# Performance work log

Hardware: AMD Instinct MI355X
Metric: run time of the kernel (lower is better)

## Reference

```python
import jax, jax.numpy as jnp
import numpy as np

GAMMA = 1.4
EX = jnp.array([1.0, 0.0], dtype=jnp.float32)
EY = jnp.array([0.0, 1.0], dtype=jnp.float32)


def _mlp(x, Ws, bs):
    h = x
    for W, b in zip(Ws[:-1], bs[:-1]):
        h = jnp.tanh(h @ W + b)
    return h @ Ws[-1] + bs[-1]


def setup_inputs() -> dict:
    key = jax.random.key(0)
    ks = jax.random.split(key, 24)
    N, NB = 32768, 4096
    inp = {}
    dom = jnp.array([1.5, 1.0], dtype=jnp.float32)
    inp['x_train'] = jax.random.uniform(ks[0], (N, 2), dtype=jnp.float32) * dom
    inp['x_inlet'] = jax.random.uniform(ks[1], (NB, 2), dtype=jnp.float32) * dom
    inp['U_inlet'] = jax.random.normal(ks[2], (NB, 4), dtype=jnp.float32)
    inp['x_base'] = jax.random.uniform(ks[3], (NB, 2), dtype=jnp.float32) * dom
    inp['x_top'] = jax.random.uniform(ks[4], (NB, 2), dtype=jnp.float32) * dom
    inp['x_slipNormal'] = jax.random.uniform(ks[5], (NB, 2), dtype=jnp.float32) * dom
    dims = [2, 128, 128, 128, 128, 4]
    for i in range(5):
        fan_in = dims[i]
        inp[f'W{i}'] = jax.random.normal(ks[6 + i], (dims[i], dims[i + 1]), dtype=jnp.float32) / jnp.sqrt(jnp.float32(fan_in))
        inp[f'b{i}'] = jnp.zeros((dims[i + 1],), dtype=jnp.float32)
    d2 = [2, 64, 64, 1]
    for i in range(3):
        inp[f'V{i}'] = jax.random.normal(ks[12 + i], (d2[i], d2[i + 1]), dtype=jnp.float32) / jnp.sqrt(jnp.float32(d2[i]))
        inp[f'c{i}'] = jnp.zeros((d2[i + 1],), dtype=jnp.float32)
    return inp


def reference(x_train, x_inlet, U_inlet, x_base, x_top, x_slipNormal,
              W0, b0, W1, b1, W2, b2, W3, b3, W4, b4,
              V0, c0, V1, c1, V2, c2):
    Ws = [W0, W1, W2, W3, W4]
    bs = [b0, b1, b2, b3, b4]
    Vs = [V0, V1, V2]
    cs = [c0, c1, c2]

    def fields(xy):
        # per-point: returns [U1..U4, f1..f4, g1..g4] (12,)
        rho, p, u, v = _mlp(xy, Ws, bs)
        E = p / (GAMMA - 1.0) + 0.5 * rho * (u * u + v * v)
        return jnp.stack([
            rho, rho * u, rho * v, E,                               # U
            rho * u, rho * u * u + p, rho * u * v, u * (E + p),     # f (x-flux)
            rho * v, rho * u * v, rho * v * v + p, v * (E + p)])    # g (y-flux)

    def dUx(xy):
        return jax.jvp(fields, (xy,), (EX,))[1][:4]

    def dUy(xy):
        return jax.jvp(fields, (xy,), (EY,))[1][:4]

    def point_residual(xy):
        _, dx = jax.jvp(fields, (xy,), (EX,))   # x-derivs of all 12 fields
        _, dy = jax.jvp(fields, (xy,), (EY,))   # y-derivs
        U_xx = jax.jvp(dUx, (xy,), (EX,))[1]    # second derivs (fwd-over-fwd)
        U_yy = jax.jvp(dUy, (xy,), (EY,))[1]
        mu = 0.01 * _mlp(xy, Vs, cs)[0] ** 2
        res = dx[4:8] + dy[8:12] - mu * (U_xx + U_yy)  # (4,)
        return res, mu

    res, mu = jax.vmap(point_residual)(x_train)  # res: (N,4), mu: (N,)
    physics = jnp.sum(jnp.mean(res ** 2, axis=0))  # r1+r2+r3+r4

    out_in = _mlp(x_inlet, Ws, bs)
    inlet = jnp.sum(jnp.mean((out_in - U_inlet) ** 2, axis=0))

    base = jnp.mean(_mlp(x_base, Ws, bs)[:, 3] ** 2)
    top = jnp.mean(_mlp(x_top, Ws, bs)[:, 3] ** 2)

    ang = -jnp.pi / 18.0
    o = _mlp(x_slipNormal, Ws, bs)
    slip = jnp.mean((-o[:, 2] * jnp.sin(ang) + o[:, 3] * jnp.cos(ang)) ** 2)

    total = physics + 10.0 * (inlet + base + top + slip) + 0.1 * jnp.mean(mu ** 2)
    return total
```

## Files before the change

kernel.cpp:

```cpp
#include <hip/hip_runtime.h>

#define NTRAIN 32768
#define NBDY   4096
#define PHYS_BLOCKS (NTRAIN / 16)
#define BDY_BLOCKS  512

typedef _Float16 f16x8 __attribute__((ext_vector_type(8)));
typedef __fp16   fp16x2 __attribute__((ext_vector_type(2)));
typedef float    f32x4 __attribute__((ext_vector_type(4)));

union FragU { uint4 q; f16x8 b; _Float16 e[8]; };
union F4  { float4 v; float f[4]; };
union U2h { _Float16 e[4]; uint2 d; };
union H2  { fp16x2 h; _Float16 e[2]; unsigned int u; };

__device__ __forceinline__ float fast_tanh(float z) {
    float e = __expf(2.0f * z);
    return 1.0f - 2.0f * __builtin_amdgcn_rcpf(e + 1.0f);
}

__device__ __forceinline__ unsigned int pk2(float a, float b) {
    H2 r; r.h = __builtin_amdgcn_cvt_pkrtz(a, b);
    return r.u;
}

__global__ __launch_bounds__(256) void pack_w_kernel(
    const float* __restrict__ W1, const float* __restrict__ W2,
    const float* __restrict__ W3, const float* __restrict__ V1,
    const float* __restrict__ W4,
    unsigned short* __restrict__ wsU, float* __restrict__ out)
{
    int b = blockIdx.x;
    if (b < 24) {
        int mat = b >> 3, rb = b & 7;
        const float* W = (mat == 0) ? W1 : (mat == 1) ? W2 : W3;
        unsigned int* hiU = (unsigned int*)(wsU + mat * 32768);
        unsigned int* loU = hiU + 8192;
        int n   = threadIdx.x & 127;
        int pr0 = threadIdx.x >> 7;
        #pragma unroll
        for (int it = 0; it < 4; it++) {
            int pr = pr0 + 2 * it;
            int k  = rb * 16 + pr * 2;
            float v0 = W[k * 128 + n];
            float v1 = W[(k + 1) * 128 + n];
            H2 hh, ll;
            hh.e[0] = (_Float16)v0;
            hh.e[1] = (_Float16)v1;
            ll.e[0] = (_Float16)(v0 - (float)hh.e[0]);
            ll.e[1] = (_Float16)(v1 - (float)hh.e[1]);
            int base = ((n >> 4) * 4 + (k >> 5)) * 64 + ((k >> 3) & 3) * 16 + (n & 15);
            int uoff = base * 4 + ((k & 7) >> 1);
            hiU[uoff] = hh.u;
            loU[uoff] = ll.u;
        }
    } else if (b == 24) {
        unsigned int* hiU = (unsigned int*)(wsU + 98304);
        int n   = threadIdx.x & 63;
        int pr0 = threadIdx.x >> 6;
        #pragma unroll
        for (int it = 0; it < 8; it++) {
            int pr = pr0 + 4 * it;
            int k  = pr * 2;
            float v0 = V1[k * 64 + n];
            float v1 = V1[(k + 1) * 64 + n];
            H2 hh;
            hh.e[0] = (_Float16)v0;
            hh.e[1] = (_Float16)v1;
            int base = ((n >> 4) * 2 + (k >> 5)) * 64 + ((k >> 3) & 3) * 16 + (n & 15);
            hiU[base * 4 + ((k & 7) >> 1)] = hh.u;
        }
        if (threadIdx.x == 0) out[0] = 0.f;
    } else {
        _Float16* hi = (_Float16*)(wsU + 102400);
        _Float16* lo = hi + 2048;
        int u4 = threadIdx.x;
        int lane = u4 & 63, ks = u4 >> 6;
        int m  = lane & 15;
        int kb = ks * 32 + ((lane >> 4) << 3);
        FragU fh, fl;
        #pragma unroll
        for (int j = 0; j < 8; j++) {
            float v = (m < 4) ? W4[(kb + j) * 4 + m] : 0.f;
            _Float16 h = (_Float16)v;
            fh.e[j] = h;
            fl.e[j] = (_Float16)(v - (float)h);
        }
        *(uint4*)(hi + u4 * 8) = fh.q;
        *(uint4*)(lo + u4 * 8) = fl.q;
    }
}

__global__ __launch_bounds__(256, 6) void fused_kernel(
    const float* __restrict__ xt,
    const float* __restrict__ x_inlet, const float* __restrict__ U_inlet,
    const float* __restrict__ x_base,  const float* __restrict__ x_top,
    const float* __restrict__ x_slip,
    const float* __restrict__ W0, const float* __restrict__ b0,
    const float* __restrict__ W1, const float* __restrict__ b1,
    const float* __restrict__ W2, const float* __restrict__ b2,
    const float* __restrict__ W3, const float* __restrict__ b3,
    const float* __restrict__ W4, const float* __restrict__ b4,
    const float* __restrict__ V0, const float* __restrict__ c0,
    const float* __restrict__ V1, const float* __restrict__ c1,
    const float* __restrict__ V2, const float* __restrict__ c2,
    const unsigned short* __restrict__ wsU,
    float* __restrict__ out)
{
    __shared__ float SM[5008];
    const int t = threadIdx.x;
    const int wv   = t >> 6;
    const int lane = t & 63;
    const int nn   = lane & 15;
    const int q    = lane >> 4;

    if (blockIdx.x < PHYS_BLOCKS) {
        unsigned short* AhU = (unsigned short*)SM;
        float* OUTF  = SM + 4352;
        float* MUV   = SM + 4608;
        float* BIASF = SM + 4624;
        unsigned short* MUhU  = AhU;
        unsigned short* MU2hU = AhU + 1152;

        const int p = t >> 4;
        const int c = t & 15;

        const int ptIdx = blockIdx.x * 16 + p;
        const float2 xy = *(const float2*)(xt + ptIdx * 2);
        const float x = xy.x, y = xy.y;

        if (t < 128) {
            BIASF[t]       = b1[t];
            BIASF[128 + t] = b2[t];
            BIASF[256 + t] = b3[t];
        }

        {
            F4 va, vb, cc;
            va.v = *(const float4*)(V0 + c * 4);
            vb.v = *(const float4*)(V0 + 64 + c * 4);
            cc.v = *(const float4*)(c0 + c * 4);
            float t0 = fast_tanh(x * va.f[0] + y * vb.f[0] + cc.f[0]);
            float t1 = fast_tanh(x * va.f[1] + y * vb.f[1] + cc.f[1]);
            float t2 = fast_tanh(x * va.f[2] + y * vb.f[2] + cc.f[2]);
            float t3 = fast_tanh(x * va.f[3] + y * vb.f[3] + cc.f[3]);
            uint2 d = make_uint2(pk2(t0, t1), pk2(t2, t3));
            *(uint2*)(MUhU + p * 72 + c * 4) = d;
        }
        __syncthreads();

        {
            f32x4 macc = {0.f, 0.f, 0.f, 0.f};
            #pragma unroll
            for (int ks = 0; ks < 2; ks++) {
                FragU mh, vh;
                mh.q = *(const uint4*)(MUhU + nn * 72 + ks * 32 + q * 8);
                vh.q = *(const uint4*)(wsU + 98304 + (((wv * 2 + ks) * 64 + lane) << 3));
                macc = __builtin_amdgcn_mfma_f32_16x16x32_f16(vh.b, mh.b, macc, 0, 0, 0);
            }
            int u2base = wv * 16 + q * 4;
            F4 cv; cv.v = *(const float4*)(c1 + u2base);
            float t0 = fast_tanh(macc[0] + cv.f[0]);
            float t1 = fast_tanh(macc[1] + cv.f[1]);
            float t2 = fast_tanh(macc[2] + cv.f[2]);
            float t3 = fast_tanh(macc[3] + cv.f[3]);
            uint2 d = make_uint2(pk2(t0, t1), pk2(t2, t3));
            *(uint2*)(MU2hU + nn * 72 + u2base) = d;
        }
        __syncthreads();

        if (t < 64) {
            int pt = t & 15, kg = t >> 4;
            float partial = 0.f;
            int base = pt * 72 + kg * 16;
            #pragma unroll
            for (int g = 0; g < 4; g++) {
                U2h hh;
                hh.d = *(const uint2*)(MU2hU + base + g * 4);
                F4 w; w.v = *(const float4*)(V2 + kg * 16 + g * 4);
                #pragma unroll
                for (int e = 0; e < 4; e++)
                    partial += (float)hh.e[e] * w.f[e];
            }
            partial += __shfl_down(partial, 32);
            partial += __shfl_down(partial, 16);
            if (t < 16) {
                float s = partial + c2[0];
                MUV[t] = 0.01f * s * s;
            }
        }
        __syncthreads();

        {
            float vals[4][8];
            #pragma unroll
            for (int j = 0; j < 8; j++) {
                int u = c * 8 + j;
                float w0 = W0[u], w1 = W0[128 + u];
                float zv = x * w0 + y * w1 + b0[u];
                float tt = fast_tanh(zv);
                float s2 = 1.f - tt * tt;
                float m2 = -2.f * tt * s2;
                vals[0][j] = tt;
                vals[1][j] = s2 * w0;
                vals[2][j] = s2 * w1;
                vals[3][j] = m2 * (w0 * w0 + w1 * w1);
            }
            #pragma unroll
            for (int s = 0; s < 4; s++) {
                uint4 d = make_uint4(pk2(vals[s][0], vals[s][1]),
                                     pk2(vals[s][2], vals[s][3]),
                                     pk2(vals[s][4], vals[s][5]),
                                     pk2(vals[s][6], vals[s][7]));
                *(uint4*)(AhU + (s * 16 + p) * 136 + c * 8) = d;
            }
        }
        __syncthreads();

        #pragma unroll 1
        for (int l = 0; l < 3; l++) {
            const unsigned short* WpL = wsU + l * 32768;
            f32x4 acc[2][4];
            #pragma unroll
            for (int i = 0; i < 2; i++)
                #pragma unroll
                for (int s = 0; s < 4; s++) {
                    acc[i][s][0] = 0.f; acc[i][s][1] = 0.f;
                    acc[i][s][2] = 0.f; acc[i][s][3] = 0.f;
                }
            #pragma unroll
            for (int ks = 0; ks < 4; ks++) {
                FragU bh[4];
                #pragma unroll
                for (int s = 0; s < 4; s++)
                    bh[s].q = *(const uint4*)(AhU + (s * 16 + nn) * 136 + ks * 32 + q * 8);
                FragU wh[2], wl[2];
                #pragma unroll
                for (int i = 0; i < 2; i++) {
                    const unsigned short* base =
                        WpL + ((((2 * wv + i) * 4 + ks) * 64 + lane) << 3);
                    wh[i].q = *(const uint4*)base;
                    wl[i].q = *(const uint4*)(base + 16384);
                }
                #pragma unroll
                for (int i = 0; i < 2; i++)
                    #pragma unroll
                    for (int s = 0; s < 4; s++) {
                        acc[i][s] = __builtin_amdgcn_mfma_f32_16x16x32_f16(
                            wh[i].b, bh[s].b, acc[i][s], 0, 0, 0);
                        acc[i][s] = __builtin_amdgcn_mfma_f32_16x16x32_f16(
                            wl[i].b, bh[s].b, acc[i][s], 0, 0, 0);
                    }
            }
            __syncthreads();
            #pragma unroll
            for (int i = 0; i < 2; i++) {
                int ubase = (2 * wv + i) * 16 + q * 4;
                F4 bv; bv.v = *(const float4*)&BIASF[l * 128 + ubase];
                float vals[4][4];
                #pragma unroll
                for (int r = 0; r < 4; r++) {
                    float z  = acc[i][0][r] + bv.f[r];
                    float zx = acc[i][1][r], zy = acc[i][2][r];
                    float zl = acc[i][3][r];
                    float tt = fast_tanh(z);
                    float s2 = 1.f - tt * tt;
                    float m2 = -2.f * tt * s2;
                    vals[0][r] = tt;
                    vals[1][r] = s2 * zx;
                    vals[2][r] = s2 * zy;
                    vals[3][r] = s2 * zl + m2 * (zx * zx + zy * zy);
                }
                #pragma unroll
                for (int s = 0; s < 4; s++) {
                    uint2 d = make_uint2(pk2(vals[s][0], vals[s][1]),
                                         pk2(vals[s][2], vals[s][3]));
                    *(uint2*)(AhU + (s * 16 + nn) * 136 + ubase) = d;
                }
            }
            __syncthreads();
        }

        {
            const unsigned short* W4p = wsU + 102400;
            f32x4 a4 = {0.f, 0.f, 0.f, 0.f};
            #pragma unroll
            for (int ks = 0; ks < 4; ks++) {
                FragU bh, wh, wl;
                bh.q = *(const uint4*)(AhU + (wv * 16 + nn) * 136 + ks * 32 + q * 8);
                const unsigned short* base = W4p + ((ks * 64 + lane) << 3);
                wh.q = *(const uint4*)base;
                wl.q = *(const uint4*)(base + 2048);
                a4 = __builtin_amdgcn_mfma_f32_16x16x32_f16(wh.b, bh.b, a4, 0, 0, 0);
                a4 = __builtin_amdgcn_mfma_f32_16x16x32_f16(wl.b, bh.b, a4, 0, 0, 0);
            }
            if (q == 0) {
                float4 o = make_float4(a4[0], a4[1], a4[2], a4[3]);
                if (wv == 0) {
                    o.x += b4[0]; o.y += b4[1]; o.z += b4[2]; o.w += b4[3];
                }
                *(float4*)&OUTF[(wv * 16 + nn) * 4] = o;
            }
        }
        __syncthreads();

        float contrib = 0.f;
        if (t < 16) {
            const int pp = t;
            const float* V   = &OUTF[(0  + pp) * 4];
            const float* DX  = &OUTF[(16 + pp) * 4];
            const float* DY  = &OUTF[(32 + pp) * 4];
            const float* LAP = &OUTF[(48 + pp) * 4];
            float r = V[0],  P = V[1],  u = V[2],  v = V[3];
            float rx = DX[0], Px = DX[1], ux = DX[2], vx = DX[3];
            float ry = DY[0], Py = DY[1], uy = DY[2], vy = DY[3];
            float rl = LAP[0], Pl = LAP[1], ul = LAP[2], vl = LAP[3];
            const float GI = 2.5f;

            float q2 = u * u + v * v;
            float E  = P * GI + 0.5f * r * q2;
            float Ex = Px * GI + 0.5f * rx * q2 + r * (u * ux + v * vx);
            float Ey = Py * GI + 0.5f * ry * q2 + r * (u * uy + v * vy);
            float EpP = E + P;

            float f1x = rx * u + r * ux;
            float f2x = rx * u * u + 2.f * r * u * ux + Px;
            float f3x = rx * u * v + r * ux * v + r * u * vx;
            float f4x = ux * EpP + u * (Ex + Px);

            float g1y = ry * v + r * vy;
            float g2y = ry * u * v + r * uy * v + r * u * vy;
            float g3y = ry * v * v + 2.f * r * v * vy + Py;
            float g4y = vy * EpP + v * (Ey + Py);

            float qx  = 2.f * (u * ux + v * vx);
            float qy  = 2.f * (u * uy + v * vy);
            float ql  = 2.f * (ux * ux + uy * uy + vx * vx + vy * vy)
                      + 2.f * (u * ul + v * vl);

            float U1s = rl;
            float U2s = rl * u + 2.f * (rx * ux + ry * uy) + r * ul;
            float U3s = rl * v + 2.f * (rx * vx + ry * vy) + r * vl;
            float U4s = Pl * GI
                      + 0.5f * (rl * q2 + 2.f * (rx * qx + ry * qy) + r * ql);

            float mu = MUV[pp];
            float r1 = f1x + g1y - mu * U1s;
            float r2 = f2x + g2y - mu * U2s;
            float r3 = f3x + g3y - mu * U3s;
            float r4 = f4x + g4y - mu * U4s;

            contrib = (r1 * r1 + r2 * r2 + r3 * r3 + r4 * r4 + 0.1f * mu * mu)
                      * (1.0f / (float)NTRAIN);
        }
        if (t < 64) {
            contrib += __shfl_down(contrib, 32);
            contrib += __shfl_down(contrib, 16);
            contrib += __shfl_down(contrib, 8);
            contrib += __shfl_down(contrib, 4);
            contrib += __shfl_down(contrib, 2);
            contrib += __shfl_down(contrib, 1);
            if (t == 0) atomicAdd(out, contrib);
        }
    } else {
        unsigned short* ShU = (unsigned short*)SM;
        float* OUTB  = SM + 2176;
        float* BIASB = SM + 2304;

        const int bb    = blockIdx.x - PHYS_BLOCKS;
        const int batch = bb >> 7;
        const int lb    = bb & 127;
        const float* xs = (batch == 0) ? x_inlet
                        : (batch == 1) ? x_base
                        : (batch == 2) ? x_top : x_slip;
        const int base_pt = lb * 32;

        {
            int p2 = t & 31, ug = t >> 5;
            float2 xy = *(const float2*)(xs + (base_pt + p2) * 2);
            float x = xy.x, y = xy.y;
            #pragma unroll
            for (int g = 0; g < 4; g++) {
                int u0 = ug * 16 + g * 4;
                F4 wa, wb, bbv;
                wa.v  = *(const float4*)(W0 + u0);
                wb.v  = *(const float4*)(W0 + 128 + u0);
                bbv.v = *(const float4*)(b0 + u0);
                float t0 = fast_tanh(x * wa.f[0] + y * wb.f[0] + bbv.f[0]);
                float t1 = fast_tanh(x * wa.f[1] + y * wb.f[1] + bbv.f[1]);
                float t2 = fast_tanh(x * wa.f[2] + y * wb.f[2] + bbv.f[2]);
                float t3 = fast_tanh(x * wa.f[3] + y * wb.f[3] + bbv.f[3]);
                uint2 d = make_uint2(pk2(t0, t1), pk2(t2, t3));
                *(uint2*)(ShU + p2 * 136 + u0) = d;
            }
            if (t < 128) {
                BIASB[t]       = b1[t];
                BIASB[128 + t] = b2[t];
                BIASB[256 + t] = b3[t];
            }
        }
        __syncthreads();

        #pragma unroll 1
        for (int l = 0; l < 3; l++) {
            const unsigned short* WpL = wsU + l * 32768;
            f32x4 acc[2][2];
            #pragma unroll
            for (int i = 0; i < 2; i++)
                #pragma unroll
                for (int n = 0; n < 2; n++) {
                    acc[i][n][0] = 0.f; acc[i][n][1] = 0.f;
                    acc[i][n][2] = 0.f; acc[i][n][3] = 0.f;
                }
            #pragma unroll
            for (int ks = 0; ks < 4; ks++) {
                FragU bh[2];
                #pragma unroll
                for (int n = 0; n < 2; n++)
                    bh[n].q = *(const uint4*)(ShU + (n * 16 + nn) * 136 + ks * 32 + q * 8);
                FragU wh[2], wl[2];
                #pragma unroll
                for (int i = 0; i < 2; i++) {
                    const unsigned short* base =
                        WpL + ((((2 * wv + i) * 4 + ks) * 64 + lane) << 3);
                    wh[i].q = *(const uint4*)base;
                    wl[i].q = *(const uint4*)(base + 16384);
                }
                #pragma unroll
                for (int i = 0; i < 2; i++)
                    #pragma unroll
                    for (int n = 0; n < 2; n++) {
                        acc[i][n] = __builtin_amdgcn_mfma_f32_16x16x32_f16(
                            wh[i].b, bh[n].b, acc[i][n], 0, 0, 0);
                        acc[i][n] = __builtin_amdgcn_mfma_f32_16x16x32_f16(
                            wl[i].b, bh[n].b, acc[i][n], 0, 0, 0);
                    }
            }
            __syncthreads();
            #pragma unroll
            for (int i = 0; i < 2; i++) {
                int ubase = (2 * wv + i) * 16 + q * 4;
                F4 bv; bv.v = *(const float4*)&BIASB[l * 128 + ubase];
                #pragma unroll
                for (int n = 0; n < 2; n++) {
                    float t0 = fast_tanh(acc[i][n][0] + bv.f[0]);
                    float t1 = fast_tanh(acc[i][n][1] + bv.f[1]);
                    float t2 = fast_tanh(acc[i][n][2] + bv.f[2]);
                    float t3 = fast_tanh(acc[i][n][3] + bv.f[3]);
                    uint2 d = make_uint2(pk2(t0, t1), pk2(t2, t3));
                    *(uint2*)(ShU + (n * 16 + nn) * 136 + ubase) = d;
                }
            }
            __syncthreads();
        }

        if (wv < 2) {
            const unsigned short* W4p = wsU + 102400;
            f32x4 a4 = {0.f, 0.f, 0.f, 0.f};
            #pragma unroll
            for (int ks = 0; ks < 4; ks++) {
                FragU bh, wh, wl;
                bh.q = *(const uint4*)(ShU + (wv * 16 + nn) * 136 + ks * 32 + q * 8);
                const unsigned short* base = W4p + ((ks * 64 + lane) << 3);
                wh.q = *(const uint4*)base;
                wl.q = *(const uint4*)(base + 2048);
                a4 = __builtin_amdgcn_mfma_f32_16x16x32_f16(wh.b, bh.b, a4, 0, 0, 0);
                a4 = __builtin_amdgcn_mfma_f32_16x16x32_f16(wl.b, bh.b, a4, 0, 0, 0);
            }
            if (q == 0) {
                float4 o = make_float4(a4[0] + b4[0], a4[1] + b4[1],
                                       a4[2] + b4[2], a4[3] + b4[3]);
                *(float4*)&OUTB[(wv * 16 + nn) * 4] = o;
            }
        }
        __syncthreads();

        float contrib = 0.f;
        if (t < 32) {
            float o0 = OUTB[t * 4 + 0], o1 = OUTB[t * 4 + 1];
            float o2 = OUTB[t * 4 + 2], o3 = OUTB[t * 4 + 3];
            float l;
            if (batch == 0) {
                float4 Ui = *(const float4*)(U_inlet + (base_pt + t) * 4);
                float d0 = o0 - Ui.x, d1 = o1 - Ui.y, d2 = o2 - Ui.z, d3 = o3 - Ui.w;
                l = d0 * d0 + d1 * d1 + d2 * d2 + d3 * d3;
            } else if (batch == 3) {
                const float sa = -0.17364817766693033f;
                const float ca =  0.9848077530122080f;
                float d = -o2 * sa + o3 * ca;
                l = d * d;
            } else {
                l = o3 * o3;
            }
            contrib = 10.0f * l * (1.0f / (float)NBDY);
        }
        if (t < 64) {
            contrib += __shfl_down(contrib, 16);
            contrib += __shfl_down(contrib, 8);
            contrib += __shfl_down(contrib, 4);
            contrib += __shfl_down(contrib, 2);
            contrib += __shfl_down(contrib, 1);
            if (t == 0) atomicAdd(out, contrib);
        }
    }
}

extern "C" void kernel_launch(void* const* d_in, const int* in_sizes, int n_in,
                              void* d_out, int out_size, void* d_ws, size_t ws_size,
                              hipStream_t stream) {
    const float* xt      = (const float*)d_in[0];
    const float* x_inlet = (const float*)d_in[1];
    const float* U_inlet = (const float*)d_in[2];
    const float* x_base  = (const float*)d_in[3];
    const float* x_top   = (const float*)d_in[4];
    const float* x_slip  = (const float*)d_in[5];
    const float* W0 = (const float*)d_in[6];
    const float* b0 = (const float*)d_in[7];
    const float* W1 = (const float*)d_in[8];
    const float* b1 = (const float*)d_in[9];
    const float* W2 = (const float*)d_in[10];
    const float* b2 = (const float*)d_in[11];
    const float* W3 = (const float*)d_in[12];
    const float* b3 = (const float*)d_in[13];
    const float* W4 = (const float*)d_in[14];
    const float* b4 = (const float*)d_in[15];
    const float* V0 = (const float*)d_in[16];
    const float* c0 = (const float*)d_in[17];
    const float* V1 = (const float*)d_in[18];
    const float* c1 = (const float*)d_in[19];
    const float* V2 = (const float*)d_in[20];
    const float* c2 = (const float*)d_in[21];
    float* out = (float*)d_out;
    unsigned short* wsU = (unsigned short*)d_ws;

    pack_w_kernel<<<26, 256, 0, stream>>>(W1, W2, W3, V1, W4, wsU, out);

    fused_kernel<<<PHYS_BLOCKS + BDY_BLOCKS, 256, 0, stream>>>(
        xt, x_inlet, U_inlet, x_base, x_top, x_slip,
        W0, b0, W1, b1, W2, b2, W3, b3, W4, b4,
        V0, c0, V1, c1, V2, c2, wsU, out);
}
```

Baseline: 151.7 us.

## Process 32 training points per block to reuse weight fragments across more MFMAs

Each physics block now handles 32 collocation points instead of 16, so every wave's loaded W fragments (hi/lo split) feed 8 column tiles of MFMAs instead of 4. This halves the number of physics blocks and the global weight-fragment loads per point. The mu-network output reduction moves later so it overlaps the final-layer work, removing a barrier. The cost is doubled accumulator registers and shared memory (launch bounds lowered from 6 to 4 blocks per CU), which lowers occupancy.

```diff
diff --git a/kernel.cpp b/kernel.cpp
--- a/kernel.cpp
+++ b/kernel.cpp
@@ -2,7 +2,7 @@
 
 #define NTRAIN 32768
 #define NBDY   4096
-#define PHYS_BLOCKS (NTRAIN / 16)
+#define PHYS_BLOCKS (NTRAIN / 32)
 #define BDY_BLOCKS  512
 
 typedef _Float16 f16x8 __attribute__((ext_vector_type(8)));
@@ -91,7 +91,7 @@
     }
 }
 
-__global__ __launch_bounds__(256, 6) void fused_kernel(
+__global__ __launch_bounds__(256, 4) void fused_kernel(
     const float* __restrict__ xt,
     const float* __restrict__ x_inlet, const float* __restrict__ U_inlet,
     const float* __restrict__ x_base,  const float* __restrict__ x_top,
@@ -107,95 +107,80 @@
     const unsigned short* __restrict__ wsU,
     float* __restrict__ out)
 {
-    __shared__ float SM[5008];
+    __shared__ float SM[10144];
     const int t = threadIdx.x;
     const int wv   = t >> 6;
     const int lane = t & 63;
     const int nn   = lane & 15;
     const int q    = lane >> 4;
+    const float* Bsl[3] = { b1, b2, b3 };
 
     if (blockIdx.x < PHYS_BLOCKS) {
-        unsigned short* AhU = (unsigned short*)SM;
-        float* OUTF  = SM + 4352;
-        float* MUV   = SM + 4608;
-        float* BIASF = SM + 4624;
-        unsigned short* MUhU  = AhU;
-        unsigned short* MU2hU = AhU + 1152;
-
-        const int p = t >> 4;
-        const int c = t & 15;
-
-        const int ptIdx = blockIdx.x * 16 + p;
-        const float2 xy = *(const float2*)(xt + ptIdx * 2);
+        unsigned short* AhU  = (unsigned short*)SM;
+        unsigned short* MU2U = AhU + 16896;
+        float* OUTF = SM + 9600;
+        float* MUV  = SM + 10112;
+        unsigned short* MUhU = AhU;
+
+        const int p8 = t >> 3;
+        const int g8 = t & 7;
+
+        const float2 xy = *(const float2*)(xt + (blockIdx.x * 32 + p8) * 2);
         const float x = xy.x, y = xy.y;
 
-        if (t < 128) {
-            BIASF[t]       = b1[t];
-            BIASF[128 + t] = b2[t];
-            BIASF[256 + t] = b3[t];
-        }
-
         {
-            F4 va, vb, cc;
-            va.v = *(const float4*)(V0 + c * 4);
-            vb.v = *(const float4*)(V0 + 64 + c * 4);
-            cc.v = *(const float4*)(c0 + c * 4);
-            float t0 = fast_tanh(x * va.f[0] + y * vb.f[0] + cc.f[0]);
-            float t1 = fast_tanh(x * va.f[1] + y * vb.f[1] + cc.f[1]);
-            float t2 = fast_tanh(x * va.f[2] + y * vb.f[2] + cc.f[2]);
-            float t3 = fast_tanh(x * va.f[3] + y * vb.f[3] + cc.f[3]);
-            uint2 d = make_uint2(pk2(t0, t1), pk2(t2, t3));
-            *(uint2*)(MUhU + p * 72 + c * 4) = d;
+            int u0 = g8 * 8;
+            F4 va0, va1, vb0, vb1, cc0, cc1;
+            va0.v = *(const float4*)(V0 + u0);
+            va1.v = *(const float4*)(V0 + u0 + 4);
+            vb0.v = *(const float4*)(V0 + 64 + u0);
+            vb1.v = *(const float4*)(V0 + 64 + u0 + 4);
+            cc0.v = *(const float4*)(c0 + u0);
+            cc1.v = *(const float4*)(c0 + u0 + 4);
+            float tv[8];
+            #pragma unroll
+            for (int i = 0; i < 4; i++) {
+                tv[i]     = fast_tanh(x * va0.f[i] + y * vb0.f[i] + cc0.f[i]);
+                tv[4 + i] = fast_tanh(x * va1.f[i] + y * vb1.f[i] + cc1.f[i]);
+            }
+            uint4 d = make_uint4(pk2(tv[0], tv[1]), pk2(tv[2], tv[3]),
+                                 pk2(tv[4], tv[5]), pk2(tv[6], tv[7]));
+            *(uint4*)(MUhU + p8 * 72 + u0) = d;
         }
         __syncthreads();
 
         {
-            f32x4 macc = {0.f, 0.f, 0.f, 0.f};
+            f32x4 m0 = {0.f, 0.f, 0.f, 0.f}, m1 = {0.f, 0.f, 0.f, 0.f};
             #pragma unroll
             for (int ks = 0; ks < 2; ks++) {
-                FragU mh, vh;
-                mh.q = *(const uint4*)(MUhU + nn * 72 + ks * 32 + q * 8);
+                FragU vh, ba, bb;
                 vh.q = *(const uint4*)(wsU + 98304 + (((wv * 2 + ks) * 64 + lane) << 3));
-                macc = __builtin_amdgcn_mfma_f32_16x16x32_f16(vh.b, mh.b, macc, 0, 0, 0);
-            }
-            int u2base = wv * 16 + q * 4;
-            F4 cv; cv.v = *(const float4*)(c1 + u2base);
-            float t0 = fast_tanh(macc[0] + cv.f[0]);
-            float t1 = fast_tanh(macc[1] + cv.f[1]);
-            float t2 = fast_tanh(macc[2] + cv.f[2]);
-            float t3 = fast_tanh(macc[3] + cv.f[3]);
-            uint2 d = make_uint2(pk2(t0, t1), pk2(t2, t3));
-            *(uint2*)(MU2hU + nn * 72 + u2base) = d;
+                ba.q = *(const uint4*)(MUhU + nn * 72 + ks * 32 + q * 8);
+                bb.q = *(const uint4*)(MUhU + (16 + nn) * 72 + ks * 32 + q * 8);
+                m0 = __builtin_amdgcn_mfma_f32_16x16x32_f16(vh.b, ba.b, m0, 0, 0, 0);
+                m1 = __builtin_amdgcn_mfma_f32_16x16x32_f16(vh.b, bb.b, m1, 0, 0, 0);
+            }
+            int u2 = wv * 16 + q * 4;
+            F4 cv; cv.v = *(const float4*)(c1 + u2);
+            float a0 = fast_tanh(m0[0] + cv.f[0]);
+            float a1 = fast_tanh(m0[1] + cv.f[1]);
+            float a2 = fast_tanh(m0[2] + cv.f[2]);
+            float a3 = fast_tanh(m0[3] + cv.f[3]);
+            *(uint2*)(MU2U + nn * 72 + u2) = make_uint2(pk2(a0, a1), pk2(a2, a3));
+            float b0v = fast_tanh(m1[0] + cv.f[0]);
+            float b1v = fast_tanh(m1[1] + cv.f[1]);
+            float b2v = fast_tanh(m1[2] + cv.f[2]);
+            float b3v = fast_tanh(m1[3] + cv.f[3]);
+            *(uint2*)(MU2U + (16 + nn) * 72 + u2) = make_uint2(pk2(b0v, b1v), pk2(b2v, b3v));
         }
         __syncthreads();
 
-        if (t < 64) {
-            int pt = t & 15, kg = t >> 4;
-            float partial = 0.f;
-            int base = pt * 72 + kg * 16;
-            #pragma unroll
-            for (int g = 0; g < 4; g++) {
-                U2h hh;
-                hh.d = *(const uint2*)(MU2hU + base + g * 4);
-                F4 w; w.v = *(const float4*)(V2 + kg * 16 + g * 4);
-                #pragma unroll
-                for (int e = 0; e < 4; e++)
-                    partial += (float)hh.e[e] * w.f[e];
-            }
-            partial += __shfl_down(partial, 32);
-            partial += __shfl_down(partial, 16);
-            if (t < 16) {
-                float s = partial + c2[0];
-                MUV[t] = 0.01f * s * s;
-            }
-        }
-        __syncthreads();
-
-        {
+        #pragma unroll
+        for (int half = 0; half < 2; half++) {
             float vals[4][8];
             #pragma unroll
             for (int j = 0; j < 8; j++) {
-                int u = c * 8 + j;
+                int u = g8 * 16 + half * 8 + j;
                 float w0 = W0[u], w1 = W0[128 + u];
                 float zv = x * w0 + y * w1 + b0[u];
                 float tt = fast_tanh(zv);
@@ -212,7 +197,7 @@
                                      pk2(vals[s][2], vals[s][3]),
                                      pk2(vals[s][4], vals[s][5]),
                                      pk2(vals[s][6], vals[s][7]));
-                *(uint4*)(AhU + (s * 16 + p) * 136 + c * 8) = d;
+                *(uint4*)(AhU + (s * 32 + p8) * 132 + g8 * 16 + half * 8) = d;
             }
         }
         __syncthreads();
@@ -220,20 +205,16 @@
         #pragma unroll 1
         for (int l = 0; l < 3; l++) {
             const unsigned short* WpL = wsU + l * 32768;
-            f32x4 acc[2][4];
+            f32x4 acc[2][8];
             #pragma unroll
             for (int i = 0; i < 2; i++)
                 #pragma unroll
-                for (int s = 0; s < 4; s++) {
-                    acc[i][s][0] = 0.f; acc[i][s][1] = 0.f;
-                    acc[i][s][2] = 0.f; acc[i][s][3] = 0.f;
+                for (int ct = 0; ct < 8; ct++) {
+                    acc[i][ct][0] = 0.f; acc[i][ct][1] = 0.f;
+                    acc[i][ct][2] = 0.f; acc[i][ct][3] = 0.f;
                 }
             #pragma unroll
             for (int ks = 0; ks < 4; ks++) {
-                FragU bh[4];
-                #pragma unroll
-                for (int s = 0; s < 4; s++)
-                    bh[s].q = *(const uint4*)(AhU + (s * 16 + nn) * 136 + ks * 32 + q * 8);
                 FragU wh[2], wl[2];
                 #pragma unroll
                 for (int i = 0; i < 2; i++) {
@@ -243,39 +224,48 @@
                     wl[i].q = *(const uint4*)(base + 16384);
                 }
                 #pragma unroll
-                for (int i = 0; i < 2; i++)
+                for (int ct = 0; ct < 8; ct++) {
+                    FragU bh;
+                    bh.q = *(const uint4*)(AhU + (ct * 16 + nn) * 132 + ks * 32 + q * 8);
+                    acc[0][ct] = __builtin_amdgcn_mfma_f32_16x16x32_f16(
+                        wh[0].b, bh.b, acc[0][ct], 0, 0, 0);
+                    acc[0][ct] = __builtin_amdgcn_mfma_f32_16x16x32_f16(
+                        wl[0].b, bh.b, acc[0][ct], 0, 0, 0);
+                    acc[1][ct] = __builtin_amdgcn_mfma_f32_16x16x32_f16(
+                        wh[1].b, bh.b, acc[1][ct], 0, 0, 0);
+                    acc[1][ct] = __builtin_amdgcn_mfma_f32_16x16x32_f16(
+                        wl[1].b, bh.b, acc[1][ct], 0, 0, 0);
+                }
+            }
+            __syncthreads();
+            #pragma unroll
+            for (int i = 0; i < 2; i++) {
+                int ubase = (2 * wv + i) * 16 + q * 4;
+                F4 bv; bv.v = *(const float4*)(Bsl[l] + ubase);
+                #pragma unroll
+                for (int h = 0; h < 2; h++) {
+                    int pp = nn + 16 * h;
+                    float vals[4][4];
+                    #pragma unroll
+                    for (int r = 0; r < 4; r++) {
+                        float z  = acc[i][h][r] + bv.f[r];
+                        float zx = acc[i][2 + h][r];
+                        float zy = acc[i][4 + h][r];
+                        float zl = acc[i][6 + h][r];
+                        float tt = fast_tanh(z);
+                        float s2 = 1.f - tt * tt;
+                        float m2 = -2.f * tt * s2;
+                        vals[0][r] = tt;
+                        vals[1][r] = s2 * zx;
+                        vals[2][r] = s2 * zy;
+                        vals[3][r] = s2 * zl + m2 * (zx * zx + zy * zy);
+                    }
                     #pragma unroll
                     for (int s = 0; s < 4; s++) {
-                        acc[i][s] = __builtin_amdgcn_mfma_f32_16x16x32_f16(
-                            wh[i].b, bh[s].b, acc[i][s], 0, 0, 0);
-                        acc[i][s] = __builtin_amdgcn_mfma_f32_16x16x32_f16(
-                            wl[i].b, bh[s].b, acc[i][s], 0, 0, 0);
+                        uint2 d = make_uint2(pk2(vals[s][0], vals[s][1]),
+                                             pk2(vals[s][2], vals[s][3]));
+                        *(uint2*)(AhU + (s * 32 + pp) * 132 + ubase) = d;
                     }
-            }
-            __syncthreads();
-            #pragma unroll
-            for (int i = 0; i < 2; i++) {
-                int ubase = (2 * wv + i) * 16 + q * 4;
-                F4 bv; bv.v = *(const float4*)&BIASF[l * 128 + ubase];
-                float vals[4][4];
-                #pragma unroll
-                for (int r = 0; r < 4; r++) {
-                    float z  = acc[i][0][r] + bv.f[r];
-                    float zx = acc[i][1][r], zy = acc[i][2][r];
-                    float zl = acc[i][3][r];
-                    float tt = fast_tanh(z);
-                    float s2 = 1.f - tt * tt;
-                    float m2 = -2.f * tt * s2;
-                    vals[0][r] = tt;
-                    vals[1][r] = s2 * zx;
-                    vals[2][r] = s2 * zy;
-                    vals[3][r] = s2 * zl + m2 * (zx * zx + zy * zy);
-                }
-                #pragma unroll
-                for (int s = 0; s < 4; s++) {
-                    uint2 d = make_uint2(pk2(vals[s][0], vals[s][1]),
-                                         pk2(vals[s][2], vals[s][3]));
-                    *(uint2*)(AhU + (s * 16 + nn) * 136 + ubase) = d;
                 }
             }
             __syncthreads();
@@ -283,34 +273,66 @@
 
         {
             const unsigned short* W4p = wsU + 102400;
-            f32x4 a4 = {0.f, 0.f, 0.f, 0.f};
+            f32x4 a4[2];
+            #pragma unroll
+            for (int r2 = 0; r2 < 2; r2++) {
+                a4[r2][0] = 0.f; a4[r2][1] = 0.f; a4[r2][2] = 0.f; a4[r2][3] = 0.f;
+            }
             #pragma unroll
             for (int ks = 0; ks < 4; ks++) {
-                FragU bh, wh, wl;
-                bh.q = *(const uint4*)(AhU + (wv * 16 + nn) * 136 + ks * 32 + q * 8);
+                FragU wh, wl;
                 const unsigned short* base = W4p + ((ks * 64 + lane) << 3);
                 wh.q = *(const uint4*)base;
                 wl.q = *(const uint4*)(base + 2048);
-                a4 = __builtin_amdgcn_mfma_f32_16x16x32_f16(wh.b, bh.b, a4, 0, 0, 0);
-                a4 = __builtin_amdgcn_mfma_f32_16x16x32_f16(wl.b, bh.b, a4, 0, 0, 0);
+                #pragma unroll
+                for (int r2 = 0; r2 < 2; r2++) {
+                    FragU bh;
+                    bh.q = *(const uint4*)(AhU + ((2 * wv + r2) * 16 + nn) * 132 + ks * 32 + q * 8);
+                    a4[r2] = __builtin_amdgcn_mfma_f32_16x16x32_f16(wh.b, bh.b, a4[r2], 0, 0, 0);
+                    a4[r2] = __builtin_amdgcn_mfma_f32_16x16x32_f16(wl.b, bh.b, a4[r2], 0, 0, 0);
+                }
             }
             if (q == 0) {
-                float4 o = make_float4(a4[0], a4[1], a4[2], a4[3]);
-                if (wv == 0) {
-                    o.x += b4[0]; o.y += b4[1]; o.z += b4[2]; o.w += b4[3];
-                }
-                *(float4*)&OUTF[(wv * 16 + nn) * 4] = o;
+                #pragma unroll
+                for (int r2 = 0; r2 < 2; r2++) {
+                    int row = (2 * wv + r2) * 16 + nn;
+                    float4 o = make_float4(a4[r2][0], a4[r2][1], a4[r2][2], a4[r2][3]);
+                    if (row < 32) {
+                        o.x += b4[0]; o.y += b4[1]; o.z += b4[2]; o.w += b4[3];
+                    }
+                    *(float4*)&OUTF[row * 4] = o;
+                }
+            }
+            if (t < 128) {
+                int p = t >> 2, kg = t & 3;
+                float partial = 0.f;
+                int base = p * 72 + kg * 16;
+                #pragma unroll
+                for (int g = 0; g < 4; g++) {
+                    U2h hh;
+                    hh.d = *(const uint2*)(MU2U + base + g * 4);
+                    F4 w; w.v = *(const float4*)(V2 + kg * 16 + g * 4);
+                    #pragma unroll
+                    for (int e = 0; e < 4; e++)
+                        partial += (float)hh.e[e] * w.f[e];
+                }
+                partial += __shfl_down(partial, 2);
+                partial += __shfl_down(partial, 1);
+                if ((t & 3) == 0) {
+                    float s = partial + c2[0];
+                    MUV[p] = 0.01f * s * s;
+                }
             }
         }
         __syncthreads();
 
         float contrib = 0.f;
-        if (t < 16) {
+        if (t < 32) {
             const int pp = t;
             const float* V   = &OUTF[(0  + pp) * 4];
-            const float* DX  = &OUTF[(16 + pp) * 4];
-            const float* DY  = &OUTF[(32 + pp) * 4];
-            const float* LAP = &OUTF[(48 + pp) * 4];
+            const float* DX  = &OUTF[(32 + pp) * 4];
+            const float* DY  = &OUTF[(64 + pp) * 4];
+            const float* LAP = &OUTF[(96 + pp) * 4];
             float r = V[0],  P = V[1],  u = V[2],  v = V[3];
             float rx = DX[0], Px = DX[1], ux = DX[2], vx = DX[3];
             float ry = DY[0], Py = DY[1], uy = DY[2], vy = DY[3];
@@ -354,7 +376,6 @@
                       * (1.0f / (float)NTRAIN);
         }
         if (t < 64) {
-            contrib += __shfl_down(contrib, 32);
             contrib += __shfl_down(contrib, 16);
             contrib += __shfl_down(contrib, 8);
             contrib += __shfl_down(contrib, 4);
```

Result: slower. 161.7 us (+6.6%).
